# Optimization experiments

Hardware: AMD Instinct MI355X
Metric: run time of the kernel (lower is better)

Reference implementation:

```python
import jax, jax.numpy as jnp
import numpy as np

EMBED_DIM = 1024
NUM_HEADS = 16
HEAD_DIM = EMBED_DIM // NUM_HEADS
SCALE = HEAD_DIM ** -0.5


def setup_inputs() -> dict:
    key = jax.random.key(0)
    ks = jax.random.split(key, 5)
    B, N, D = 2, 2048, EMBED_DIM
    std = D ** -0.5
    x = jax.random.normal(ks[0], (B, N, D), dtype=jnp.float32)
    W_qkv = jax.random.normal(ks[1], (D, 3 * D), dtype=jnp.float32) * std
    b_qkv = jnp.zeros((3 * D,), dtype=jnp.float32)
    W_proj = jax.random.normal(ks[2], (D, D), dtype=jnp.float32) * std
    b_proj = jnp.zeros((D,), dtype=jnp.float32)
    return {"x": x, "W_qkv": W_qkv, "b_qkv": b_qkv, "W_proj": W_proj, "b_proj": b_proj}


def reference(x, W_qkv, b_qkv, W_proj, b_proj):
    B, N, D = x.shape
    H, Hd = NUM_HEADS, HEAD_DIM
    qkv = x @ W_qkv + b_qkv                      # (B, N, 3D)
    qkv = qkv.reshape(B, N, 3, H, Hd)
    q = qkv[:, :, 0].transpose(0, 2, 1, 3)       # (B, H, N, Hd)
    k = qkv[:, :, 1].transpose(0, 2, 1, 3)
    v = qkv[:, :, 2].transpose(0, 2, 1, 3)
    attn = jnp.einsum('bhqd,bhkd->bhqk', q, k) * SCALE  # (B, H, N, N)
    attn = jax.nn.softmax(attn, axis=-1)
    out = jnp.einsum('bhqk,bhkd->bhqd', attn, v)        # (B, H, N, Hd)
    out = out.transpose(0, 2, 1, 3).reshape(B, N, D)
    return out @ W_proj + b_proj
```

## Files before the change

### kernel.cpp

```cpp
#include <hip/hip_runtime.h>
#include <stdint.h>

#define BATCH 2
#define NH 16
#define SEQ 2048
#define DIM 1024
#define HD 64
#define MROWS (BATCH*SEQ)

typedef __attribute__((ext_vector_type(8))) _Float16 f16x8;
typedef __attribute__((ext_vector_type(16))) float f32x16;
typedef __attribute__((ext_vector_type(4))) float f32x4;
typedef __attribute__((ext_vector_type(2))) __fp16 fp16x2;
typedef __attribute__((ext_vector_type(4))) short short4v;

__device__ __forceinline__ short f2h(float f) {
  union { _Float16 h; short s; } u;
  u.h = (_Float16)f;
  return u.s;
}

__device__ __forceinline__ float fast_exp2(float x) {
#if __has_builtin(__builtin_amdgcn_exp2f)
  return __builtin_amdgcn_exp2f(x);
#else
  return exp2f(x);
#endif
}

__device__ __forceinline__ unsigned pk2(float a, float b) {
  union { fp16x2 h; unsigned u; } x;
  x.h = __builtin_amdgcn_cvt_pkrtz(a, b);
  return x.u;
}

__device__ __forceinline__ void perm32swap(unsigned &a, unsigned &b) {
  unsigned as = (unsigned)__shfl_xor((int)a, 32);
  unsigned bs = (unsigned)__shfl_xor((int)b, 32);
  bool lo = ((threadIdx.x & 63) < 32);
  unsigned na = lo ? a : bs;
  unsigned nb = lo ? as : b;
  a = na; b = nb;
}

__device__ __forceinline__ void async_load16(const void* g, void* l) {
  __builtin_amdgcn_global_load_lds((const __attribute__((address_space(1))) void*)g,
                                   (__attribute__((address_space(3))) void*)l, 16, 0, 0);
}

__global__ __launch_bounds__(256) void k_cvt(const float* __restrict__ in,
                                             short* __restrict__ out, int n4) {
  int i = blockIdx.x * 256 + threadIdx.x;
  if (i >= n4) return;
  float4 v = ((const float4*)in)[i];
  short4v o;
  o[0] = f2h(v.x); o[1] = f2h(v.y); o[2] = f2h(v.z); o[3] = f2h(v.w);
  ((short4v*)out)[i] = o;
}

__global__ __launch_bounds__(256) void k_transpose(const float* __restrict__ in,
                                                   short* __restrict__ out,
                                                   int K, int N) {
  __shared__ float t[32][33];
  int n0 = blockIdx.x * 32, k0 = blockIdx.y * 32;
  int tx = threadIdx.x, ty = threadIdx.y;
  #pragma unroll
  for (int i = 0; i < 32; i += 8)
    t[ty + i][tx] = in[(size_t)(k0 + ty + i) * N + (n0 + tx)];
  __syncthreads();
  #pragma unroll
  for (int i = 0; i < 32; i += 8)
    out[(size_t)(n0 + ty + i) * K + (k0 + tx)] = f2h(t[tx][ty + i]);
}

template <int MODE, int BM>
__global__ __launch_bounds__(256) void k_gemm_bt(
    const short* __restrict__ A, const short* __restrict__ Bt,
    const float* __restrict__ bias,
    short* __restrict__ Qd, short* __restrict__ Kd, short* __restrict__ Vtd,
    float* __restrict__ Cf, int Ncols, int Kdim) {
  constexpr int BN = 128, BK = 64;
  constexpr int RI = BM / 32;
  __shared__ short Al[2][BM * BK];
  __shared__ short Bl[2][BN * BK];
  const int tid = threadIdx.x;
  const int lane = tid & 63;
  const int wid = tid >> 6;
  const int wr = wid >> 1, wc = wid & 1;
  const int m0 = blockIdx.y * BM, n0 = blockIdx.x * BN;
  const int l15 = lane & 15, lk = (lane >> 4) * 8;

  f32x4 acc[RI][4] = {};

  auto stage = [&](int kt, int buf) {
    int k0 = kt * BK;
    #pragma unroll
    for (int i2 = 0; i2 < BM / 32; i2++) {
      int c = i2 * 256 + tid;
      int r = c >> 3, cs = (c & 7) * 8;
      async_load16(A + (size_t)(m0 + r) * Kdim + k0 + (cs ^ ((r & 7) * 8)),
                   &Al[buf][c * 8]);
    }
    #pragma unroll
    for (int i2 = 0; i2 < 4; i2++) {
      int c = i2 * 256 + tid;
      int r = c >> 3, cs = (c & 7) * 8;
      async_load16(Bt + (size_t)(n0 + r) * Kdim + k0 + (cs ^ ((r & 7) * 8)),
                   &Bl[buf][c * 8]);
    }
  };

  auto compute = [&](int buf) {
    f16x8 af[2][RI], bfr[2][4];
    #pragma unroll
    for (int kk = 0; kk < 2; kk++) {
      #pragma unroll
      for (int i = 0; i < RI; i++) {
        int row = wr * (BM / 2) + i * 16 + l15;
        af[kk][i] = *(const f16x8*)&Al[buf][row * 64 + ((kk * 32 + lk) ^ ((row & 7) * 8))];
      }
      #pragma unroll
      for (int j = 0; j < 4; j++) {
        int row = wc * 64 + j * 16 + l15;
        bfr[kk][j] = *(const f16x8*)&Bl[buf][row * 64 + ((kk * 32 + lk) ^ ((row & 7) * 8))];
      }
    }
    __builtin_amdgcn_s_setprio(1);
    #pragma unroll
    for (int i = 0; i < RI; i++)
      #pragma unroll
      for (int j = 0; j < 4; j++) {
        acc[i][j] = __builtin_amdgcn_mfma_f32_16x16x32_f16(af[0][i], bfr[0][j], acc[i][j], 0, 0, 0);
        acc[i][j] = __builtin_amdgcn_mfma_f32_16x16x32_f16(af[1][i], bfr[1][j], acc[i][j], 0, 0, 0);
      }
    __builtin_amdgcn_s_setprio(0);
  };

  stage(0, 0);
  const int NT = Kdim / BK;
  for (int t = 0; t < NT; t++) {
    int cur = t & 1;
    if (t + 1 < NT) {
      stage(t + 1, cur ^ 1);
      if constexpr (BM == 128) asm volatile("s_waitcnt vmcnt(8)" ::: "memory");
      else                     asm volatile("s_waitcnt vmcnt(6)" ::: "memory");
    } else {
      asm volatile("s_waitcnt vmcnt(0)" ::: "memory");
    }
    __builtin_amdgcn_s_barrier();
    __builtin_amdgcn_sched_barrier(0);
    compute(cur);
    __builtin_amdgcn_sched_barrier(0);
    __builtin_amdgcn_s_barrier();
  }

  const int rl = (lane >> 4) * 4;
  if (MODE == 0) {
    #pragma unroll
    for (int j = 0; j < 4; j++) {
      int col = n0 + wc * 64 + j * 16 + l15;
      float bv = bias[col];
      int sec = col >> 10;
      int cc = col & 1023;
      int h = cc >> 6, hd = cc & 63;
      float mul = (sec == 0) ? (0.125f * 1.44269504088896f) : 1.0f;
      #pragma unroll
      for (int i = 0; i < RI; i++) {
        int rowb = m0 + wr * (BM / 2) + i * 16 + rl;
        #pragma unroll
        for (int r = 0; r < 4; r++) {
          int row = rowb + r;
          int b = row >> 11, nr = row & 2047;
          short v = f2h((acc[i][j][r] + bv) * mul);
          size_t bh = (size_t)(b * NH + h);
          size_t base2 = bh * (size_t)(SEQ * HD);
          if (sec == 0) {
            Qd[base2 + (size_t)nr * HD + hd] = v;
          } else if (sec == 1) {
            Kd[base2 + (size_t)(((nr >> 5) * 4 + (hd >> 4)) * 512 +
                                (((hd >> 3) & 1) * 32 + (nr & 31)) * 8 + (hd & 7))] = v;
          } else {
            Vtd[base2 + (size_t)(((nr >> 4) * 2 + (hd >> 5)) * 512 +
                                 (((nr >> 3) & 1) * 32 + (hd & 31)) * 8 + (nr & 7))] = v;
          }
        }
      }
    }
  } else {
    #pragma unroll
    for (int j = 0; j < 4; j++) {
      int col = n0 + wc * 64 + j * 16 + l15;
      float bv = bias[col];
      #pragma unroll
      for (int i = 0; i < RI; i++) {
        int rowb = m0 + wr * (BM / 2) + i * 16 + rl;
        #pragma unroll
        for (int r = 0; r < 4; r++)
          Cf[(size_t)(rowb + r) * Ncols + col] = acc[i][j][r] + bv;
      }
    }
  }
}

#define QBLK 128
#define NKVT (SEQ / 64)

#define PACK8(sv, R0, lsv, OUT) do {                                        \
    float e0_ = fast_exp2((sv)[R0 + 0]), e1_ = fast_exp2((sv)[R0 + 1]);     \
    float e2_ = fast_exp2((sv)[R0 + 2]), e3_ = fast_exp2((sv)[R0 + 3]);     \
    float e4_ = fast_exp2((sv)[R0 + 4]), e5_ = fast_exp2((sv)[R0 + 5]);     \
    float e6_ = fast_exp2((sv)[R0 + 6]), e7_ = fast_exp2((sv)[R0 + 7]);     \
    lsv += ((e0_ + e1_) + (e2_ + e3_)) + ((e4_ + e5_) + (e6_ + e7_));       \
    unsigned u0_ = pk2(e0_, e1_), u1_ = pk2(e2_, e3_);                      \
    unsigned u2_ = pk2(e4_, e5_), u3_ = pk2(e6_, e7_);                      \
    perm32swap(u0_, u2_);                                                   \
    perm32swap(u1_, u3_);                                                   \
    union { unsigned u[4]; f16x8 v; } W_;                                   \
    W_.u[0] = u0_; W_.u[1] = u1_; W_.u[2] = u2_; W_.u[3] = u3_;             \
    OUT = W_.v;                                                             \
  } while (0)

__global__ __launch_bounds__(256) void k_flash(const short* __restrict__ Qd,
                                               const short* __restrict__ KB,
                                               const short* __restrict__ VB,
                                               short* __restrict__ Od) {
  __shared__ short Kl[2][4096];
  __shared__ short Vl[2][4096];
  const int tid = threadIdx.x;
  const int lane = tid & 63;
  const int w = tid >> 6;
  const int l31 = lane & 31, lh = lane >> 5;
  const int bh = blockIdx.x;
  const int q0 = blockIdx.y * QBLK + w * 32;
  const size_t base = (size_t)bh * (size_t)(SEQ * HD);

  f16x8 qf[4];
  #pragma unroll
  for (int ds = 0; ds < 4; ds++)
    qf[ds] = *(const f16x8*)(Qd + base + (size_t)(q0 + l31) * HD + ds * 16 + lh * 8);

  f32x16 o[2] = {};
  float lsum = 0.f;

#define STAGE(kvt, buf) do {                                                \
    const short* ks_ = KB + base + (size_t)(kvt) * 4096;                    \
    const short* vs_ = VB + base + (size_t)(kvt) * 4096;                    \
    async_load16(ks_ + tid * 8, &Kl[buf][tid * 8]);                         \
    async_load16(ks_ + (tid + 256) * 8, &Kl[buf][(tid + 256) * 8]);         \
    async_load16(vs_ + tid * 8, &Vl[buf][tid * 8]);                         \
    async_load16(vs_ + (tid + 256) * 8, &Vl[buf][(tid + 256) * 8]);         \
  } while (0)

  auto compute = [&](int cur) {
    f16x8 kf0[4], kf1[4];
    #pragma unroll
    for (int ds = 0; ds < 4; ds++) {
      kf0[ds] = *(const f16x8*)&Kl[cur][(ds * 64 + lane) * 8];
      kf1[ds] = *(const f16x8*)&Kl[cur][((4 + ds) * 64 + lane) * 8];
    }
    f32x16 sA = {}, sB = {};
    __builtin_amdgcn_s_setprio(1);
    #pragma unroll
    for (int ds = 0; ds < 4; ds++) {
      sA = __builtin_amdgcn_mfma_f32_32x32x16_f16(kf0[ds], qf[ds], sA, 0, 0, 0);
      sB = __builtin_amdgcn_mfma_f32_32x32x16_f16(kf1[ds], qf[ds], sB, 0, 0, 0);
    }
    __builtin_amdgcn_s_setprio(0);
    f16x8 vf[4][2];
    #pragma unroll
    for (int ks = 0; ks < 4; ks++)
      #pragma unroll
      for (int hdt = 0; hdt < 2; hdt++)
        vf[ks][hdt] = *(const f16x8*)&Vl[cur][((ks * 2 + hdt) * 64 + lane) * 8];
    f16x8 p[4];
    PACK8(sA, 0, lsum, p[0]); PACK8(sA, 8, lsum, p[1]);
    PACK8(sB, 0, lsum, p[2]); PACK8(sB, 8, lsum, p[3]);
    __builtin_amdgcn_s_setprio(1);
    #pragma unroll
    for (int ks = 0; ks < 4; ks++) {
      o[0] = __builtin_amdgcn_mfma_f32_32x32x16_f16(p[ks], vf[ks][0], o[0], 0, 0, 0);
      o[1] = __builtin_amdgcn_mfma_f32_32x32x16_f16(p[ks], vf[ks][1], o[1], 0, 0, 0);
    }
    __builtin_amdgcn_s_setprio(0);
  };

  STAGE(0, 0);
  for (int kvt = 0; kvt < NKVT; kvt++) {
    int cur = kvt & 1;
    if (kvt + 1 < NKVT) {
      STAGE(kvt + 1, cur ^ 1);
      asm volatile("s_waitcnt vmcnt(4)" ::: "memory");
    } else {
      asm volatile("s_waitcnt vmcnt(0)" ::: "memory");
    }
    __builtin_amdgcn_s_barrier();
    __builtin_amdgcn_sched_barrier(0);
    compute(cur);
    __builtin_amdgcn_sched_barrier(0);
    __builtin_amdgcn_s_barrier();
  }
#undef STAGE

  lsum += __shfl_xor(lsum, 32);
  float inv = 1.f / lsum;

  const int b = bh >> 4, h = bh & 15;
  #pragma unroll
  for (int reg = 0; reg < 16; reg++) {
    int qrow = (reg & 3) + 8 * (reg >> 2) + 4 * lh;
    float s = __shfl(inv, qrow);
    size_t r0 = (size_t)(b * SEQ + q0 + qrow) * DIM + h * 64;
    Od[r0 + l31]      = f2h(o[0][reg] * s);
    Od[r0 + 32 + l31] = f2h(o[1][reg] * s);
  }
}

extern "C" void kernel_launch(void* const* d_in, const int* in_sizes, int n_in,
                              void* d_out, int out_size, void* d_ws, size_t ws_size,
                              hipStream_t stream) {
  const float* x     = (const float*)d_in[0];
  const float* Wqkv  = (const float*)d_in[1];
  const float* bqkv  = (const float*)d_in[2];
  const float* Wproj = (const float*)d_in[3];
  const float* bproj = (const float*)d_in[4];
  float* out = (float*)d_out;

  char* ws = (char*)d_ws;
  short* x_h    = (short*)(ws);
  short* Wqkv_t = (short*)(ws + ((size_t)8  << 20));
  short* Wproj_t= (short*)(ws + ((size_t)14 << 20));
  short* Qd     = (short*)(ws + ((size_t)16 << 20));
  short* Kd     = (short*)(ws + ((size_t)24 << 20));
  short* Vtd    = (short*)(ws + ((size_t)32 << 20));
  short* Od     = (short*)(ws + ((size_t)40 << 20));

  k_cvt<<<(MROWS * DIM / 4 + 255) / 256, 256, 0, stream>>>(x, x_h, MROWS * DIM / 4);
  dim3 tb(32, 8);
  k_transpose<<<dim3(3 * DIM / 32, DIM / 32), tb, 0, stream>>>(Wqkv, Wqkv_t, DIM, 3 * DIM);
  k_transpose<<<dim3(DIM / 32, DIM / 32), tb, 0, stream>>>(Wproj, Wproj_t, DIM, DIM);
  k_gemm_bt<0, 128><<<dim3(3 * DIM / 128, MROWS / 128), 256, 0, stream>>>(
      x_h, Wqkv_t, bqkv, Qd, Kd, Vtd, nullptr, 3 * DIM, DIM);
  k_flash<<<dim3(BATCH * NH, SEQ / QBLK), 256, 0, stream>>>(Qd, Kd, Vtd, Od);
  k_gemm_bt<1, 64><<<dim3(DIM / 128, MROWS / 64), 256, 0, stream>>>(
      Od, Wproj_t, bproj, nullptr, nullptr, nullptr, out, DIM, DIM);
}
```

Before: 133.7 us.

## Split KV sequence across two wave groups in flash kernel and use permlane32 swap

```diff
diff --git a/kernel.cpp b/kernel.cpp
--- a/kernel.cpp
+++ b/kernel.cpp
@@ -13,6 +13,7 @@
 typedef __attribute__((ext_vector_type(4))) float f32x4;
 typedef __attribute__((ext_vector_type(2))) __fp16 fp16x2;
 typedef __attribute__((ext_vector_type(4))) short short4v;
+typedef __attribute__((ext_vector_type(2))) unsigned uint2v;
 
 __device__ __forceinline__ short f2h(float f) {
   union { _Float16 h; short s; } u;
@@ -35,12 +36,17 @@
 }
 
 __device__ __forceinline__ void perm32swap(unsigned &a, unsigned &b) {
+#if __has_builtin(__builtin_amdgcn_permlane32_swap)
+  uint2v r = __builtin_amdgcn_permlane32_swap(a, b, false, false);
+  a = r[0]; b = r[1];
+#else
   unsigned as = (unsigned)__shfl_xor((int)a, 32);
   unsigned bs = (unsigned)__shfl_xor((int)b, 32);
   bool lo = ((threadIdx.x & 63) < 32);
   unsigned na = lo ? a : bs;
   unsigned nb = lo ? as : b;
   a = na; b = nb;
+#endif
 }
 
 __device__ __forceinline__ void async_load16(const void* g, void* l) {
@@ -203,7 +209,7 @@
 }
 
 #define QBLK 128
-#define NKVT (SEQ / 64)
+#define NSTEP (SEQ / 128)
 
 #define PACK8(sv, R0, lsv, OUT) do {                                        \
     float e0_ = fast_exp2((sv)[R0 + 0]), e1_ = fast_exp2((sv)[R0 + 1]);     \
@@ -220,18 +226,21 @@
     OUT = W_.v;                                                             \
   } while (0)
 
-__global__ __launch_bounds__(256) void k_flash(const short* __restrict__ Qd,
-                                               const short* __restrict__ KB,
-                                               const short* __restrict__ VB,
-                                               short* __restrict__ Od) {
-  __shared__ short Kl[2][4096];
-  __shared__ short Vl[2][4096];
+__global__ __launch_bounds__(512, 4) void k_flash(const short* __restrict__ Qd,
+                                                  const short* __restrict__ KB,
+                                                  const short* __restrict__ VB,
+                                                  short* __restrict__ Od) {
+  __shared__ short Kl[2][2][4096];
+  __shared__ short Vl[2][2][4096];
   const int tid = threadIdx.x;
   const int lane = tid & 63;
   const int w = tid >> 6;
+  const int wq = w & 3;
+  const int grp = tid >> 8;
+  const int gtid = tid & 255;
   const int l31 = lane & 31, lh = lane >> 5;
   const int bh = blockIdx.x;
-  const int q0 = blockIdx.y * QBLK + w * 32;
+  const int q0 = blockIdx.y * QBLK + wq * 32;
   const size_t base = (size_t)bh * (size_t)(SEQ * HD);
 
   f16x8 qf[4];
@@ -242,21 +251,21 @@
   f32x16 o[2] = {};
   float lsum = 0.f;
 
-#define STAGE(kvt, buf) do {                                                \
-    const short* ks_ = KB + base + (size_t)(kvt) * 4096;                    \
-    const short* vs_ = VB + base + (size_t)(kvt) * 4096;                    \
-    async_load16(ks_ + tid * 8, &Kl[buf][tid * 8]);                         \
-    async_load16(ks_ + (tid + 256) * 8, &Kl[buf][(tid + 256) * 8]);         \
-    async_load16(vs_ + tid * 8, &Vl[buf][tid * 8]);                         \
-    async_load16(vs_ + (tid + 256) * 8, &Vl[buf][(tid + 256) * 8]);         \
+#define STAGE(kvt, buf) do {                                                 \
+    const short* ks_ = KB + base + (size_t)(kvt) * 4096;                     \
+    const short* vs_ = VB + base + (size_t)(kvt) * 4096;                     \
+    async_load16(ks_ + gtid * 8, &Kl[grp][buf][gtid * 8]);                   \
+    async_load16(ks_ + (gtid + 256) * 8, &Kl[grp][buf][(gtid + 256) * 8]);   \
+    async_load16(vs_ + gtid * 8, &Vl[grp][buf][gtid * 8]);                   \
+    async_load16(vs_ + (gtid + 256) * 8, &Vl[grp][buf][(gtid + 256) * 8]);   \
   } while (0)
 
   auto compute = [&](int cur) {
     f16x8 kf0[4], kf1[4];
     #pragma unroll
     for (int ds = 0; ds < 4; ds++) {
-      kf0[ds] = *(const f16x8*)&Kl[cur][(ds * 64 + lane) * 8];
-      kf1[ds] = *(const f16x8*)&Kl[cur][((4 + ds) * 64 + lane) * 8];
+      kf0[ds] = *(const f16x8*)&Kl[grp][cur][(ds * 64 + lane) * 8];
+      kf1[ds] = *(const f16x8*)&Kl[grp][cur][((4 + ds) * 64 + lane) * 8];
     }
     f32x16 sA = {}, sB = {};
     __builtin_amdgcn_s_setprio(1);
@@ -271,7 +280,7 @@
     for (int ks = 0; ks < 4; ks++)
       #pragma unroll
       for (int hdt = 0; hdt < 2; hdt++)
-        vf[ks][hdt] = *(const f16x8*)&Vl[cur][((ks * 2 + hdt) * 64 + lane) * 8];
+        vf[ks][hdt] = *(const f16x8*)&Vl[grp][cur][((ks * 2 + hdt) * 64 + lane) * 8];
     f16x8 p[4];
     PACK8(sA, 0, lsum, p[0]); PACK8(sA, 8, lsum, p[1]);
     PACK8(sB, 0, lsum, p[2]); PACK8(sB, 8, lsum, p[3]);
@@ -284,11 +293,11 @@
     __builtin_amdgcn_s_setprio(0);
   };
 
-  STAGE(0, 0);
-  for (int kvt = 0; kvt < NKVT; kvt++) {
-    int cur = kvt & 1;
-    if (kvt + 1 < NKVT) {
-      STAGE(kvt + 1, cur ^ 1);
+  STAGE(grp, 0);
+  for (int step = 0; step < NSTEP; step++) {
+    int cur = step & 1;
+    if (step + 1 < NSTEP) {
+      STAGE(2 * (step + 1) + grp, cur ^ 1);
       asm volatile("s_waitcnt vmcnt(4)" ::: "memory");
     } else {
       asm volatile("s_waitcnt vmcnt(0)" ::: "memory");
@@ -301,17 +310,43 @@
   }
 #undef STAGE
 
-  lsum += __shfl_xor(lsum, 32);
-  float inv = 1.f / lsum;
-
-  const int b = bh >> 4, h = bh & 15;
-  #pragma unroll
-  for (int reg = 0; reg < 16; reg++) {
-    int qrow = (reg & 3) + 8 * (reg >> 2) + 4 * lh;
-    float s = __shfl(inv, qrow);
-    size_t r0 = (size_t)(b * SEQ + q0 + qrow) * DIM + h * 64;
-    Od[r0 + l31]      = f2h(o[0][reg] * s);
-    Od[r0 + 32 + l31] = f2h(o[1][reg] * s);
+  float* mb = (float*)&Kl[0][0][0];
+  float* reg0 = mb + wq * 2112;
+  if (grp == 1) {
+    #pragma unroll
+    for (int hdt = 0; hdt < 2; hdt++)
+      #pragma unroll
+      for (int rq = 0; rq < 4; rq++) {
+        f32x4 v4;
+        v4[0] = o[hdt][rq * 4 + 0]; v4[1] = o[hdt][rq * 4 + 1];
+        v4[2] = o[hdt][rq * 4 + 2]; v4[3] = o[hdt][rq * 4 + 3];
+        *(f32x4*)&reg0[(hdt * 4 + rq) * 256 + lane * 4] = v4;
+      }
+    reg0[2048 + lane] = lsum;
+  }
+  __syncthreads();
+  if (grp == 0) {
+    #pragma unroll
+    for (int hdt = 0; hdt < 2; hdt++)
+      #pragma unroll
+      for (int rq = 0; rq < 4; rq++) {
+        f32x4 v4 = *(const f32x4*)&reg0[(hdt * 4 + rq) * 256 + lane * 4];
+        o[hdt][rq * 4 + 0] += v4[0]; o[hdt][rq * 4 + 1] += v4[1];
+        o[hdt][rq * 4 + 2] += v4[2]; o[hdt][rq * 4 + 3] += v4[3];
+      }
+    lsum += reg0[2048 + lane];
+
+    lsum += __shfl_xor(lsum, 32);
+    float inv = 1.f / lsum;
+    const int b = bh >> 4, h = bh & 15;
+    #pragma unroll
+    for (int reg = 0; reg < 16; reg++) {
+      int qrow = (reg & 3) + 8 * (reg >> 2) + 4 * lh;
+      float s = __shfl(inv, qrow);
+      size_t r0 = (size_t)(b * SEQ + q0 + qrow) * DIM + h * 64;
+      Od[r0 + l31]      = f2h(o[0][reg] * s);
+      Od[r0 + 32 + l31] = f2h(o[1][reg] * s);
+    }
   }
 }
 
@@ -340,7 +375,7 @@
   k_transpose<<<dim3(DIM / 32, DIM / 32), tb, 0, stream>>>(Wproj, Wproj_t, DIM, DIM);
   k_gemm_bt<0, 128><<<dim3(3 * DIM / 128, MROWS / 128), 256, 0, stream>>>(
       x_h, Wqkv_t, bqkv, Qd, Kd, Vtd, nullptr, 3 * DIM, DIM);
-  k_flash<<<dim3(BATCH * NH, SEQ / QBLK), 256, 0, stream>>>(Qd, Kd, Vtd, Od);
+  k_flash<<<dim3(BATCH * NH, SEQ / QBLK), 512, 0, stream>>>(Qd, Kd, Vtd, Od);
   k_gemm_bt<1, 64><<<dim3(DIM / 128, MROWS / 64), 256, 0, stream>>>(
       Od, Wproj_t, bproj, nullptr, nullptr, nullptr, out, DIM, DIM);
 }
```

Result: slower. 143.7 us (+7.5%).

## Split KV tile across wave pairs in flash kernel and use permlane32 swap

Applied to the files above, without the earlier changes.

```diff
diff --git a/kernel.cpp b/kernel.cpp
--- a/kernel.cpp
+++ b/kernel.cpp
@@ -13,6 +13,7 @@
 typedef __attribute__((ext_vector_type(4))) float f32x4;
 typedef __attribute__((ext_vector_type(2))) __fp16 fp16x2;
 typedef __attribute__((ext_vector_type(4))) short short4v;
+typedef __attribute__((ext_vector_type(2))) unsigned uint2v;
 
 __device__ __forceinline__ short f2h(float f) {
   union { _Float16 h; short s; } u;
@@ -35,12 +36,17 @@
 }
 
 __device__ __forceinline__ void perm32swap(unsigned &a, unsigned &b) {
+#if __has_builtin(__builtin_amdgcn_permlane32_swap)
+  uint2v r = __builtin_amdgcn_permlane32_swap(a, b, false, false);
+  a = r[0]; b = r[1];
+#else
   unsigned as = (unsigned)__shfl_xor((int)a, 32);
   unsigned bs = (unsigned)__shfl_xor((int)b, 32);
   bool lo = ((threadIdx.x & 63) < 32);
   unsigned na = lo ? a : bs;
   unsigned nb = lo ? as : b;
   a = na; b = nb;
+#endif
 }
 
 __device__ __forceinline__ void async_load16(const void* g, void* l) {
@@ -202,7 +208,7 @@
   }
 }
 
-#define QBLK 128
+#define QBLK 64
 #define NKVT (SEQ / 64)
 
 #define PACK8(sv, R0, lsv, OUT) do {                                        \
@@ -229,9 +235,11 @@
   const int tid = threadIdx.x;
   const int lane = tid & 63;
   const int w = tid >> 6;
+  const int wq = w >> 1;
+  const int kvh = w & 1;
   const int l31 = lane & 31, lh = lane >> 5;
   const int bh = blockIdx.x;
-  const int q0 = blockIdx.y * QBLK + w * 32;
+  const int q0 = blockIdx.y * QBLK + wq * 32;
   const size_t base = (size_t)bh * (size_t)(SEQ * HD);
 
   f16x8 qf[4];
@@ -252,32 +260,27 @@
   } while (0)
 
   auto compute = [&](int cur) {
-    f16x8 kf0[4], kf1[4];
-    #pragma unroll
-    for (int ds = 0; ds < 4; ds++) {
-      kf0[ds] = *(const f16x8*)&Kl[cur][(ds * 64 + lane) * 8];
-      kf1[ds] = *(const f16x8*)&Kl[cur][((4 + ds) * 64 + lane) * 8];
-    }
-    f32x16 sA = {}, sB = {};
+    f16x8 kf[4];
+    #pragma unroll
+    for (int ds = 0; ds < 4; ds++)
+      kf[ds] = *(const f16x8*)&Kl[cur][((kvh * 4 + ds) * 64 + lane) * 8];
+    f32x16 s = {};
     __builtin_amdgcn_s_setprio(1);
     #pragma unroll
-    for (int ds = 0; ds < 4; ds++) {
-      sA = __builtin_amdgcn_mfma_f32_32x32x16_f16(kf0[ds], qf[ds], sA, 0, 0, 0);
-      sB = __builtin_amdgcn_mfma_f32_32x32x16_f16(kf1[ds], qf[ds], sB, 0, 0, 0);
-    }
+    for (int ds = 0; ds < 4; ds++)
+      s = __builtin_amdgcn_mfma_f32_32x32x16_f16(kf[ds], qf[ds], s, 0, 0, 0);
     __builtin_amdgcn_s_setprio(0);
-    f16x8 vf[4][2];
-    #pragma unroll
-    for (int ks = 0; ks < 4; ks++)
+    f16x8 vf[2][2];
+    #pragma unroll
+    for (int ks = 0; ks < 2; ks++)
       #pragma unroll
       for (int hdt = 0; hdt < 2; hdt++)
-        vf[ks][hdt] = *(const f16x8*)&Vl[cur][((ks * 2 + hdt) * 64 + lane) * 8];
-    f16x8 p[4];
-    PACK8(sA, 0, lsum, p[0]); PACK8(sA, 8, lsum, p[1]);
-    PACK8(sB, 0, lsum, p[2]); PACK8(sB, 8, lsum, p[3]);
+        vf[ks][hdt] = *(const f16x8*)&Vl[cur][(((kvh * 2 + ks) * 2 + hdt) * 64 + lane) * 8];
+    f16x8 p[2];
+    PACK8(s, 0, lsum, p[0]); PACK8(s, 8, lsum, p[1]);
     __builtin_amdgcn_s_setprio(1);
     #pragma unroll
-    for (int ks = 0; ks < 4; ks++) {
+    for (int ks = 0; ks < 2; ks++) {
       o[0] = __builtin_amdgcn_mfma_f32_32x32x16_f16(p[ks], vf[ks][0], o[0], 0, 0, 0);
       o[1] = __builtin_amdgcn_mfma_f32_32x32x16_f16(p[ks], vf[ks][1], o[1], 0, 0, 0);
     }
@@ -301,17 +304,43 @@
   }
 #undef STAGE
 
-  lsum += __shfl_xor(lsum, 32);
-  float inv = 1.f / lsum;
-
-  const int b = bh >> 4, h = bh & 15;
-  #pragma unroll
-  for (int reg = 0; reg < 16; reg++) {
-    int qrow = (reg & 3) + 8 * (reg >> 2) + 4 * lh;
-    float s = __shfl(inv, qrow);
-    size_t r0 = (size_t)(b * SEQ + q0 + qrow) * DIM + h * 64;
-    Od[r0 + l31]      = f2h(o[0][reg] * s);
-    Od[r0 + 32 + l31] = f2h(o[1][reg] * s);
+  float* ob = (float*)&Kl[0][0];
+  float* lb = (float*)&Vl[0][0];
+  if (kvh == 1) {
+    #pragma unroll
+    for (int hdt = 0; hdt < 2; hdt++)
+      #pragma unroll
+      for (int rq = 0; rq < 4; rq++) {
+        f32x4 v4;
+        v4[0] = o[hdt][rq * 4 + 0]; v4[1] = o[hdt][rq * 4 + 1];
+        v4[2] = o[hdt][rq * 4 + 2]; v4[3] = o[hdt][rq * 4 + 3];
+        *(f32x4*)&ob[wq * 2048 + (hdt * 4 + rq) * 256 + lane * 4] = v4;
+      }
+    lb[wq * 64 + lane] = lsum;
+  }
+  __syncthreads();
+  if (kvh == 0) {
+    #pragma unroll
+    for (int hdt = 0; hdt < 2; hdt++)
+      #pragma unroll
+      for (int rq = 0; rq < 4; rq++) {
+        f32x4 v4 = *(const f32x4*)&ob[wq * 2048 + (hdt * 4 + rq) * 256 + lane * 4];
+        o[hdt][rq * 4 + 0] += v4[0]; o[hdt][rq * 4 + 1] += v4[1];
+        o[hdt][rq * 4 + 2] += v4[2]; o[hdt][rq * 4 + 3] += v4[3];
+      }
+    lsum += lb[wq * 64 + lane];
+
+    lsum += __shfl_xor(lsum, 32);
+    float inv = 1.f / lsum;
+    const int b = bh >> 4, h = bh & 15;
+    #pragma unroll
+    for (int reg = 0; reg < 16; reg++) {
+      int qrow = (reg & 3) + 8 * (reg >> 2) + 4 * lh;
+      float s = __shfl(inv, qrow);
+      size_t r0 = (size_t)(b * SEQ + q0 + qrow) * DIM + h * 64;
+      Od[r0 + l31]      = f2h(o[0][reg] * s);
+      Od[r0 + 32 + l31] = f2h(o[1][reg] * s);
+    }
   }
 }
 
```

New measurement: 139.4 us. 1.04x slower.
